# Optimization experiments

Hardware: AMD Instinct MI355X
Metric: run time of the kernel (lower is better)

The kernel has to match this reference:

```python
import jax, jax.numpy as jnp
import numpy as np

NUM_EXPERTS = 8
TOP_K = 2
RANK = 16
LORA_ALPHA = 32
SCALING = LORA_ALPHA / RANK  # 2.0


def setup_inputs() -> dict:
    key = jax.random.key(0)
    ks = jax.random.split(key, 6)
    B, S, D_IN, D_OUT = 4, 2048, 4096, 4096
    x = jax.random.normal(ks[0], (B, S, D_IN), dtype=jnp.float32)
    W_base = jax.random.normal(ks[1], (D_OUT, D_IN), dtype=jnp.float32) * 0.02
    b_base = jax.random.normal(ks[2], (D_OUT,), dtype=jnp.float32) * 0.02
    W_router = jax.random.normal(ks[3], (NUM_EXPERTS, D_IN), dtype=jnp.float32) * 0.02
    A = jax.random.normal(ks[4], (NUM_EXPERTS, RANK, D_IN), dtype=jnp.float32) * 0.02
    Bm = jax.random.normal(ks[5], (D_OUT, RANK), dtype=jnp.float32) * 0.02
    Bm = jnp.broadcast_to(Bm, (NUM_EXPERTS, D_OUT, RANK)) * jnp.arange(1, NUM_EXPERTS + 1, dtype=jnp.float32)[:, None, None] * 0.2
    return {"x": x, "W_base": W_base, "b_base": b_base, "W_router": W_router, "A": A, "B": Bm}


def reference(x, W_base, b_base, W_router, A, B):
    bs, seq, d_in = x.shape
    T = bs * seq
    xf = x.reshape(T, d_in)  # flatten tokens, as in torch .view(-1, d_in)

    # base linear layer
    base = xf @ W_base.T + b_base  # [T, d_out]

    # local router: logits -> top-k -> softmax over selected weights
    logits = xf @ W_router.T                      # [T, E]
    rw, sel = jax.lax.top_k(logits, TOP_K)        # [T, K] each
    rw = jax.nn.softmax(rw, axis=-1)              # router_norm == 'softmax'

    # per-token per-expert combine weight (zero for unselected experts);
    # mathematically identical to gather-LoRA-scatter since top-k experts
    # per token are distinct.
    onehot = jax.nn.one_hot(sel, NUM_EXPERTS, dtype=rw.dtype)  # [T, K, E]
    w = jnp.einsum('tk,tke->te', rw, onehot)                   # [T, E]

    # LoRA: down-project to tiny rank, weight, then up-project; contract
    # expert+rank together to avoid a [T, E, d_out] intermediate.
    h = jnp.einsum('td,erd->ter', xf, A)          # [T, E, r] (small)
    lora = jnp.einsum('ter,te,eor->to', h, w, B) * SCALING  # [T, d_out]

    return (base + lora).reshape(bs, seq, -1)
```

## Files before the change

### kernel.cpp

```cpp
#include <hip/hip_runtime.h>
#include <hip/hip_bf16.h>
#include <stdint.h>

#define T_TOKENS 8192
#define DIN      4096
#define DOUT     4096
#define NE       8
#define RANK     16
#define KEXT     128
#define KTOT     4224
#define NS       132
#define SCALING  2.0f

typedef __attribute__((ext_vector_type(8))) short   short8;
typedef __attribute__((ext_vector_type(4))) float   float4v;

__device__ __forceinline__ unsigned short f2bf(float f) {
    union { float f; unsigned int u; } c; c.f = f;
    unsigned int u = c.u;
    u += 0x7FFFu + ((u >> 16) & 1u);
    return (unsigned short)(u >> 16);
}

#define GLD_LDS(g, l) __builtin_amdgcn_global_load_lds( \
    (const __attribute__((address_space(1))) void*)(g), \
    (__attribute__((address_space(3))) void*)(l), 16, 0, 0)

__global__ __launch_bounds__(256) void k_front(const float* __restrict__ x,
                                               const float* __restrict__ Wr,
                                               const float* __restrict__ Wb,
                                               const float* __restrict__ A,
                                               const float* __restrict__ Bm,
                                               unsigned short* __restrict__ xa,
                                               unsigned short* __restrict__ Wa,
                                               unsigned short* __restrict__ Acat,
                                               float* __restrict__ w8) {
    __shared__ float lds_wr[8 * 1024];
    int b = blockIdx.x;
    int tid = threadIdx.x;

    if (b < 2048) {
        int l = tid & 63, w = tid >> 6;
        int t = b * 4 + w;
        const float4* x4 = (const float4*)x;
        const float4* Wr4 = (const float4*)Wr;
        unsigned short* xarow = xa + (size_t)t * KTOT;

        float racc[NE];
#pragma unroll
        for (int e = 0; e < NE; e++) racc[e] = 0.f;

        for (int ci = 0; ci < 4; ci++) {
            __syncthreads();
#pragma unroll
            for (int jj = 0; jj < 8; jj++) {
                int f = jj * 256 + tid;
                int e = f >> 8, col = f & 255;
                *(float4*)&lds_wr[f * 4] = Wr4[e * 1024 + ci * 256 + col];
            }
            __syncthreads();
            float4 xv[4];
#pragma unroll
            for (int j = 0; j < 4; j++)
                xv[j] = x4[(size_t)t * 1024 + ci * 256 + j * 64 + l];
#pragma unroll
            for (int j = 0; j < 4; j++) {
                ushort4 p;
                p.x = f2bf(xv[j].x); p.y = f2bf(xv[j].y);
                p.z = f2bf(xv[j].z); p.w = f2bf(xv[j].w);
                *(ushort4*)(xarow + (ci * 256 + j * 64 + l) * 4) = p;
            }
#pragma unroll
            for (int e = 0; e < NE; e++) {
#pragma unroll
                for (int j = 0; j < 4; j++) {
                    float4 wv = *(const float4*)&lds_wr[(e * 256 + j * 64 + l) * 4];
                    racc[e] += xv[j].x * wv.x + xv[j].y * wv.y + xv[j].z * wv.z + xv[j].w * wv.w;
                }
            }
        }
#pragma unroll
        for (int e = 0; e < NE; e++) {
            float v = racc[e];
#pragma unroll
            for (int off = 32; off > 0; off >>= 1) v += __shfl_xor(v, off);
            racc[e] = v;
        }
        if (l == 0) {
            int e0 = 0;
#pragma unroll
            for (int e = 1; e < NE; e++) if (racc[e] > racc[e0]) e0 = e;
            int e1 = -1;
#pragma unroll
            for (int e = 0; e < NE; e++)
                if (e != e0 && (e1 < 0 || racc[e] > racc[e1])) e1 = e;
            float a1 = __expf(racc[e1] - racc[e0]);
            float inv = 1.0f / (1.0f + a1);
            float* wrow = w8 + t * NE;
#pragma unroll
            for (int e = 0; e < NE; e++)
                wrow[e] = (e == e0) ? inv * SCALING : ((e == e1) ? a1 * inv * SCALING : 0.f);
        }
    } else if (b < 18432) {
        int idx = (b - 2048) * 256 + tid;
        float4 v = ((const float4*)Wb)[idx];
        int o  = idx >> 10;
        int kc = idx & 1023;
        ushort4 p;
        p.x = f2bf(v.x); p.y = f2bf(v.y); p.z = f2bf(v.z); p.w = f2bf(v.w);
        *(ushort4*)(Wa + (size_t)o * KTOT + kc * 4) = p;
    } else {
        int tid2 = (b - 18432) * 256 + tid;
        if (tid2 < NE * RANK * DIN) {
            Acat[tid2] = f2bf(A[tid2]);
        } else {
            int j   = tid2 - NE * RANK * DIN;
            int o   = j >> 7;
            int rem = j & 127;
            int e   = rem >> 4;
            int r   = rem & 15;
            Wa[(size_t)o * KTOT + DIN + rem] = f2bf(Bm[(size_t)e * (DOUT * RANK) + o * RANK + r]);
        }
    }
}

__global__ __launch_bounds__(256) void k_h(unsigned short* __restrict__ xa,
                                           const unsigned short* __restrict__ Acat,
                                           const float* __restrict__ w8) {
    __shared__ unsigned short lds_x[32 * 128];
    __shared__ unsigned short lds_a[128 * 128];
    int m0  = blockIdx.x * 32;
    int tid = threadIdx.x;
    int l = tid & 63, w = tid >> 6;
    int quad = l >> 4, lr = l & 15;

    float4v acc[2][2] = {};

    for (int k0 = 0; k0 < DIN; k0 += 128) {
        __syncthreads();
#pragma unroll
        for (int it = 0; it < 2; it++) {
            int c = it * 256 + tid;
            int row = c >> 4, s = c & 15;
            int kc = s ^ (row & 15);
            GLD_LDS(xa + (size_t)(m0 + row) * KTOT + k0 + kc * 8, lds_x + c * 8);
        }
#pragma unroll
        for (int it = 0; it < 8; it++) {
            int c = it * 256 + tid;
            int row = c >> 4, s = c & 15;
            int kc = s ^ (row & 15);
            GLD_LDS(Acat + (size_t)row * DIN + k0 + kc * 8, lds_a + c * 8);
        }
        __syncthreads();
#pragma unroll
        for (int kk = 0; kk < 4; kk++) {
            int kc = kk * 4 + quad;
            short8 a[2], bfr[2];
#pragma unroll
            for (int mi = 0; mi < 2; mi++) {
                int row = mi * 16 + lr;
                a[mi] = *(const short8*)&lds_x[row * 128 + ((kc ^ lr) * 8)];
            }
#pragma unroll
            for (int ni = 0; ni < 2; ni++) {
                int row = w * 32 + ni * 16 + lr;
                bfr[ni] = *(const short8*)&lds_a[row * 128 + ((kc ^ lr) * 8)];
            }
#pragma unroll
            for (int mi = 0; mi < 2; mi++)
#pragma unroll
                for (int ni = 0; ni < 2; ni++)
                    acc[mi][ni] = __builtin_amdgcn_mfma_f32_16x16x32_bf16(a[mi], bfr[ni], acc[mi][ni], 0, 0, 0);
        }
    }

#pragma unroll
    for (int mi = 0; mi < 2; mi++)
#pragma unroll
        for (int ni = 0; ni < 2; ni++) {
            int col = w * 32 + ni * 16 + lr;
            int e = col >> 4;
#pragma unroll
            for (int i = 0; i < 4; i++) {
                int t = m0 + mi * 16 + quad * 4 + i;
                float v = acc[mi][ni][i] * w8[t * NE + e];
                xa[(size_t)t * KTOT + DIN + col] = f2bf(v);
            }
        }
}

#define BAR() __builtin_amdgcn_s_barrier()
#define LGKM0() do { asm volatile("s_waitcnt lgkmcnt(0)" ::: "memory"); \
                     __builtin_amdgcn_sched_barrier(0); } while (0)
#define STAGEA6(ts, b) do { \
    const unsigned short* s_ = srcA + (size_t)(ts) * 32; \
    char* d_ = smem + (b) * 16384 + tid16; \
    GLD_LDS(s_, d_); \
    GLD_LDS(s_ + (size_t)128 * KTOT, d_ + 8192); \
} while (0)
#define STAGEB6(ts, b) do { \
    const unsigned short* s_ = srcB + (size_t)(ts) * 32; \
    char* d_ = smem + 32768 + (b) * 8192 + tid16; \
    GLD_LDS(s_, d_); \
} while (0)

__global__ __launch_bounds__(512, 4) void k_main(const unsigned short* __restrict__ xa,
                                                 const unsigned short* __restrict__ Wa,
                                                 const float* __restrict__ bias,
                                                 float* __restrict__ out) {
    __shared__ __align__(16) char smem[49152];
    int tid = threadIdx.x;
    int l = tid & 63, w = tid >> 6;
    int lr = l & 15, quad = l >> 4;
    int wm = w >> 1, wn = w & 1;

    int bid = blockIdx.x;
    int xcd = bid & 7, idx = bid >> 3;
    int bm  = (xcd & 3) * 8 + (idx & 7);
    int bn  = (xcd >> 2) * 16 + (idx >> 3);

    int laneoff = lr * 64 + ((quad ^ ((lr >> 1) & 3)) << 4);
    int amioff = wm * 4096 + laneoff;
    int bnioff = wn * 4096 + laneoff;

    int srow  = w * 16 + ((tid >> 2) & 15);
    int skq   = (tid & 3) ^ ((tid >> 3) & 3);
    int tid16 = tid * 16;
    const unsigned short* srcA = xa + (size_t)(bm * 256 + srow) * KTOT + skq * 8;
    const unsigned short* srcB = Wa + (size_t)(bn * 128 + srow) * KTOT + skq * 8;

    float4v acc[4][4] = {};
    short8 af[4], bf[4];

    STAGEA6(0, 0); STAGEB6(0, 0);
    STAGEA6(1, 1); STAGEB6(1, 1);

    for (int s = 0; s < NS; ++s) {
        int b = s & 1;
        asm volatile("s_waitcnt vmcnt(3)" ::: "memory");
        BAR();
        const char* pa = smem + b * 16384;
        const char* pb = smem + 32768 + b * 8192;
#pragma unroll
        for (int mi = 0; mi < 4; mi++)
            af[mi] = *(const short8*)(pa + amioff + mi * 1024);
#pragma unroll
        for (int ni = 0; ni < 4; ni++)
            bf[ni] = *(const short8*)(pb + bnioff + ni * 1024);
        LGKM0();
        BAR();
        int ts2 = (s + 2 < NS) ? s + 2 : NS - 1;
        STAGEA6(ts2, b); STAGEB6(ts2, b);
        __builtin_amdgcn_s_setprio(1);
#pragma unroll
        for (int mi = 0; mi < 4; mi++)
#pragma unroll
            for (int ni = 0; ni < 4; ni++)
                acc[mi][ni] = __builtin_amdgcn_mfma_f32_16x16x32_bf16(af[mi], bf[ni], acc[mi][ni], 0, 0, 0);
        __builtin_amdgcn_s_setprio(0);
    }
    asm volatile("s_waitcnt vmcnt(0) lgkmcnt(0)" ::: "memory");

    int trow0 = bm * 256 + wm * 64;
    int ocol0 = bn * 128 + wn * 64;
#pragma unroll
    for (int ni = 0; ni < 4; ni++) {
        int o = ocol0 + ni * 16 + lr;
        float bb = bias[o];
#pragma unroll
        for (int mi = 0; mi < 4; mi++) {
#pragma unroll
            for (int i = 0; i < 4; i++) {
                int trow = trow0 + mi * 16 + quad * 4 + i;
                out[(size_t)trow * DOUT + o] = acc[mi][ni][i] + bb;
            }
        }
    }
}

extern "C" void kernel_launch(void* const* d_in, const int* in_sizes, int n_in,
                              void* d_out, int out_size, void* d_ws, size_t ws_size,
                              hipStream_t stream) {
    const float* x  = (const float*)d_in[0];
    const float* Wb = (const float*)d_in[1];
    const float* bb = (const float*)d_in[2];
    const float* Wr = (const float*)d_in[3];
    const float* A  = (const float*)d_in[4];
    const float* Bm = (const float*)d_in[5];
    float* out = (float*)d_out;

    char* ws = (char*)d_ws;
    unsigned short* xa   = (unsigned short*)(ws);
    unsigned short* Wa   = (unsigned short*)(ws + 69206016);
    unsigned short* Acat = (unsigned short*)(ws + 69206016 + 34603008);
    float*          w8   = (float*)(ws + 69206016 + 34603008 + 1048576);

    k_front<<<dim3(22528), dim3(256), 0, stream>>>(x, Wr, Wb, A, Bm, xa, Wa, Acat, w8);
    k_h    <<<dim3(256),   dim3(256), 0, stream>>>(xa, Acat, w8);
    k_main <<<dim3(1024),  dim3(512), 0, stream>>>(xa, Wa, bb, out);
}
```

Before: 587.7 us.

## Halve waves per block and double per-wave M tile in main GEMM

The main GEMM block now uses 4 waves instead of 8, with each wave computing a 128x64 output tile (8x4 MFMA fragments) instead of 64x64. Staging of A and B tiles into LDS is restructured into a unified per-buffer layout, with each thread issuing six async global-to-LDS loads per stage. This raises MFMA work per LDS fragment read and cuts wave-level overhead, at the cost of more accumulator registers per wave and fewer waves available to hide latency.

```diff
diff --git a/kernel.cpp b/kernel.cpp
--- a/kernel.cpp
+++ b/kernel.cpp
@@ -193,19 +193,27 @@
 #define BAR() __builtin_amdgcn_s_barrier()
 #define LGKM0() do { asm volatile("s_waitcnt lgkmcnt(0)" ::: "memory"); \
                      __builtin_amdgcn_sched_barrier(0); } while (0)
-#define STAGEA6(ts, b) do { \
-    const unsigned short* s_ = srcA + (size_t)(ts) * 32; \
-    char* d_ = smem + (b) * 16384 + tid16; \
-    GLD_LDS(s_, d_); \
-    GLD_LDS(s_ + (size_t)128 * KTOT, d_ + 8192); \
+#define STAGE7(ts, b) do { \
+    int k0_ = (ts) * 32; \
+    _Pragma("unroll") \
+    for (int it_ = 0; it_ < 4; it_++) { \
+        int c_ = it_ * 256 + tid; \
+        int row_ = c_ >> 2; \
+        int kq_ = (c_ & 3) ^ ((c_ >> 3) & 3); \
+        GLD_LDS(xa + (size_t)(bm * 256 + row_) * KTOT + k0_ + kq_ * 8, \
+                smem + (b) * 24576 + c_ * 16); \
+    } \
+    _Pragma("unroll") \
+    for (int it_ = 0; it_ < 2; it_++) { \
+        int c_ = it_ * 256 + tid; \
+        int row_ = c_ >> 2; \
+        int kq_ = (c_ & 3) ^ ((c_ >> 3) & 3); \
+        GLD_LDS(Wa + (size_t)(bn * 128 + row_) * KTOT + k0_ + kq_ * 8, \
+                smem + (b) * 24576 + 16384 + c_ * 16); \
+    } \
 } while (0)
-#define STAGEB6(ts, b) do { \
-    const unsigned short* s_ = srcB + (size_t)(ts) * 32; \
-    char* d_ = smem + 32768 + (b) * 8192 + tid16; \
-    GLD_LDS(s_, d_); \
-} while (0)
-
-__global__ __launch_bounds__(512, 4) void k_main(const unsigned short* __restrict__ xa,
+
+__global__ __launch_bounds__(256, 2) void k_main(const unsigned short* __restrict__ xa,
                                                  const unsigned short* __restrict__ Wa,
                                                  const float* __restrict__ bias,
                                                  float* __restrict__ out) {
@@ -221,40 +229,33 @@
     int bn  = (xcd >> 2) * 16 + (idx >> 3);
 
     int laneoff = lr * 64 + ((quad ^ ((lr >> 1) & 3)) << 4);
-    int amioff = wm * 4096 + laneoff;
-    int bnioff = wn * 4096 + laneoff;
-
-    int srow  = w * 16 + ((tid >> 2) & 15);
-    int skq   = (tid & 3) ^ ((tid >> 3) & 3);
-    int tid16 = tid * 16;
-    const unsigned short* srcA = xa + (size_t)(bm * 256 + srow) * KTOT + skq * 8;
-    const unsigned short* srcB = Wa + (size_t)(bn * 128 + srow) * KTOT + skq * 8;
-
-    float4v acc[4][4] = {};
-    short8 af[4], bf[4];
-
-    STAGEA6(0, 0); STAGEB6(0, 0);
-    STAGEA6(1, 1); STAGEB6(1, 1);
+    int aoff = wm * 8192 + laneoff;
+    int boff = 16384 + wn * 4096 + laneoff;
+
+    float4v acc[8][4] = {};
+    short8 af[8], bf[4];
+
+    STAGE7(0, 0);
+    STAGE7(1, 1);
 
     for (int s = 0; s < NS; ++s) {
         int b = s & 1;
-        asm volatile("s_waitcnt vmcnt(3)" ::: "memory");
+        asm volatile("s_waitcnt vmcnt(6)" ::: "memory");
         BAR();
-        const char* pa = smem + b * 16384;
-        const char* pb = smem + 32768 + b * 8192;
-#pragma unroll
-        for (int mi = 0; mi < 4; mi++)
-            af[mi] = *(const short8*)(pa + amioff + mi * 1024);
+        const char* pbuf = smem + b * 24576;
+#pragma unroll
+        for (int mi = 0; mi < 8; mi++)
+            af[mi] = *(const short8*)(pbuf + aoff + mi * 1024);
 #pragma unroll
         for (int ni = 0; ni < 4; ni++)
-            bf[ni] = *(const short8*)(pb + bnioff + ni * 1024);
+            bf[ni] = *(const short8*)(pbuf + boff + ni * 1024);
         LGKM0();
         BAR();
         int ts2 = (s + 2 < NS) ? s + 2 : NS - 1;
-        STAGEA6(ts2, b); STAGEB6(ts2, b);
+        STAGE7(ts2, b);
         __builtin_amdgcn_s_setprio(1);
 #pragma unroll
-        for (int mi = 0; mi < 4; mi++)
+        for (int mi = 0; mi < 8; mi++)
 #pragma unroll
             for (int ni = 0; ni < 4; ni++)
                 acc[mi][ni] = __builtin_amdgcn_mfma_f32_16x16x32_bf16(af[mi], bf[ni], acc[mi][ni], 0, 0, 0);
@@ -262,14 +263,14 @@
     }
     asm volatile("s_waitcnt vmcnt(0) lgkmcnt(0)" ::: "memory");
 
-    int trow0 = bm * 256 + wm * 64;
+    int trow0 = bm * 256 + wm * 128;
     int ocol0 = bn * 128 + wn * 64;
 #pragma unroll
     for (int ni = 0; ni < 4; ni++) {
         int o = ocol0 + ni * 16 + lr;
         float bb = bias[o];
 #pragma unroll
-        for (int mi = 0; mi < 4; mi++) {
+        for (int mi = 0; mi < 8; mi++) {
 #pragma unroll
             for (int i = 0; i < 4; i++) {
                 int trow = trow0 + mi * 16 + quad * 4 + i;
@@ -298,5 +299,5 @@
 
     k_front<<<dim3(22528), dim3(256), 0, stream>>>(x, Wr, Wb, A, Bm, xa, Wa, Acat, w8);
     k_h    <<<dim3(256),   dim3(256), 0, stream>>>(xa, Acat, w8);
-    k_main <<<dim3(1024),  dim3(512), 0, stream>>>(xa, Wa, bb, out);
-}
+    k_main <<<dim3(1024),  dim3(256), 0, stream>>>(xa, Wa, bb, out);
+}
```

Measured after the change: 607.2 us. 1.03x slower.
